# Kernel optimization log

Measured on AMD Instinct MI355X. Metric: run time of the kernel, lower is better.

Reference implementation:

```python
import jax, jax.numpy as jnp
import numpy as np

N, C, T, V = 16, 128, 128, 25
K, H, OC = 3, 8, 256          # kernel_size subsets, heads, out_channels
HOPMAX = 12                   # hop values in [0, 12); emb_table size HOPMAX
EPS_BN = 1e-5
EPS_NORM = 1e-4


def setup_inputs() -> dict:
    key = jax.random.key(0)
    ks = jax.random.split(key, 12)
    s = 0.05
    x = jax.random.normal(ks[0], (N, C, T, V), jnp.float32)
    hop = jax.random.randint(ks[1], (V, V), 0, HOPMAX)
    emb_table = jax.random.normal(ks[2], (K, H, HOPMAX), jnp.float32) * s
    # A initialized as identity (as in the module) plus small noise for nontrivial grads
    A = jnp.tile(jnp.eye(V, dtype=jnp.float32), (K, H, 1, 1)) \
        + jax.random.normal(ks[3], (K, H, V, V), jnp.float32) * s
    w_block = jax.random.normal(ks[4], (K * OC, C // H), jnp.float32) * s  # grouped 1x1 conv, groups=K*H
    b_block = jax.random.normal(ks[5], (K * OC,), jnp.float32) * s
    bn_gamma = jnp.ones((OC,), jnp.float32)
    bn_beta = jnp.zeros((OC,), jnp.float32)
    res_w = jax.random.normal(ks[6], (OC, C), jnp.float32) * s  # residual 1x1 conv
    res_b = jax.random.normal(ks[7], (OC,), jnp.float32) * s
    res_bn_gamma = jnp.ones((OC,), jnp.float32)
    res_bn_beta = jnp.zeros((OC,), jnp.float32)
    return {"x": x, "hop": hop, "emb_table": emb_table, "A": A,
            "w_block": w_block, "b_block": b_block,
            "bn_gamma": bn_gamma, "bn_beta": bn_beta,
            "res_w": res_w, "res_b": res_b,
            "res_bn_gamma": res_bn_gamma, "res_bn_beta": res_bn_beta}


def _batchnorm(x, gamma, beta):
    # training-mode BatchNorm2d: batch stats over (N, T, V), biased variance
    m = jnp.mean(x, axis=(0, 2, 3), keepdims=True)
    v = jnp.var(x, axis=(0, 2, 3), keepdims=True)
    xn = (x - m) * jax.lax.rsqrt(v + EPS_BN)
    return gamma[None, :, None, None] * xn + beta[None, :, None, None]


def _l2_col_norm(w):
    # torch.norm(w, p=2, dim=-2, keepdim=True) + 1e-4  (in-degree normalization)
    return jnp.sqrt(jnp.sum(w * w, axis=-2, keepdims=True)) + EPS_NORM


def reference(x, hop, emb_table, A, w_block, b_block, bn_gamma, bn_beta,
              res_w, res_b, res_bn_gamma, res_bn_beta):
    n, c, t, v = x.shape
    # residual: 1x1 TemporalConv2d + BN (in_channels != out_channels)
    res = jnp.einsum('nctv,oc->notv', x, res_w) + res_b[None, :, None, None]
    res = _batchnorm(res, res_bn_gamma, res_bn_beta)

    # hop-embedding gather -> [K, H, V, V]; fuse normalized B and A
    B = emb_table[:, :, hop]
    BnA = B / _l2_col_norm(B) + A / _l2_col_norm(A)

    # graph conv: einsum over joint dim v (broadcast over k)
    xh = x.reshape(n, H, c // H, t, v)                      # [N,H,C/H,T,V]
    y = jnp.einsum('nhctv,khvw->nkhctw', xh, BnA)           # [N,K,H,C/H,T,V]
    y = y.reshape(n, K * H, c // H, t, v)                   # groups = K*H

    # grouped 1x1 conv: per-group [C/H -> OC/H] GEMM
    wg = w_block.reshape(K * H, OC // H, c // H)
    out = jnp.einsum('ngctv,goc->ngotv', y, wg)             # [N,K*H,OC/H,T,V]
    out = out.reshape(n, K * OC, t, v) + b_block[None, :, None, None]

    # sum over the K kernel subsets
    out = out.reshape(n, K, OC, t, v).sum(axis=1)
    out = _batchnorm(out, bn_gamma, bn_beta)
    return jax.nn.relu(out + res)
```

## Files before the change

kernel.cpp:

```cpp
#include <hip/hip_runtime.h>
#include <stdint.h>

typedef __attribute__((ext_vector_type(8))) short short8;
typedef __attribute__((ext_vector_type(4))) float f32x4;

#define B_BNA    0ull
#define B_STATS  60416ull
#define B_RESW2  64512ull
#define B_PART   130048ull
#define B_E2     1178624ull
#define B_XB     7994368ull
#define B_MAIN   21625856ull
#define B_RES    47840256ull

#define NTV 51200.0f

__device__ __forceinline__ unsigned short f2bf(float f) {
    unsigned u = __float_as_uint(f);
    return (unsigned short)((u + 0x7fffu + ((u >> 16) & 1u)) >> 16);
}
__device__ __forceinline__ float bf2f(unsigned s) { return __uint_as_float(s << 16); }

__device__ __forceinline__ float wave_sum(float v) {
#pragma unroll
    for (int m = 1; m < 64; m <<= 1) v += __shfl_xor(v, m, 64);
    return v;
}

__global__ __launch_bounds__(256) void k_prep(const int* __restrict__ hop,
                                              const float* __restrict__ emb,
                                              const float* __restrict__ A,
                                              const float* __restrict__ res_w,
                                              float* __restrict__ bna,
                                              float* __restrict__ stats,
                                              unsigned short* __restrict__ resw2) {
    int g = blockIdx.x, tid = threadIdx.x;
    if (g < 24) {
        if (tid < 25) {
            int w = tid;
            float nb = 0.f, na = 0.f;
            for (int v = 0; v < 25; v++) {
                float e = emb[g*12 + hop[v*25 + w]];
                nb += e*e;
                float a = A[((size_t)g*25 + v)*25 + w];
                na += a*a;
            }
            nb = sqrtf(nb) + 1e-4f;
            na = sqrtf(na) + 1e-4f;
            for (int v = 0; v < 25; v++) {
                float e = emb[g*12 + hop[v*25 + w]];
                float a = A[((size_t)g*25 + v)*25 + w];
                bna[g*625 + v*25 + w] = e/nb + a/na;
            }
        }
    } else if (g == 24) {
#pragma unroll
        for (int i = 0; i < 4; i++) stats[i*256 + tid] = 0.f;
    } else {
        int base = (g - 25) * 4096 + tid * 16;
#pragma unroll
        for (int j = 0; j < 16; j++) resw2[base + j] = f2bf(res_w[base + j]);
    }
}

__global__ __launch_bounds__(256) void k_prep2(const float* __restrict__ w_block,
                                               const float* __restrict__ bna,
                                               unsigned short* __restrict__ E2) {
    __shared__ float bl[3*625];
    __shared__ float wl[3*64];
    int bid = blockIdx.x;
    int half = bid & 1, og = (bid >> 1) & 7, h = bid >> 4;
    int tid = threadIdx.x;

    for (int i = tid; i < 1875; i += 256) {
        int k3 = i / 625, j = i - k3*625;
        bl[i] = bna[(k3*8 + h)*625 + j];
    }
    if (tid < 192) {
        int k3 = tid >> 6, o = (tid >> 4) & 3, c = tid & 15;
        wl[tid] = w_block[(k3*256 + h*32 + og*4 + o)*16 + c];
    }
    __syncthreads();

    unsigned short* dst = E2 + (size_t)(h*8 + og)*53248;
    int e0 = half * 26624;
    for (int e = e0 + tid; e < e0 + 26624; e += 256) {
        int kc = e >> 12;
        int n  = (e >> 5) & 127;
        int kk = e & 31;
        int k  = kc*32 + kk;
        int o  = n >> 5, w = n & 31;
        float val = 0.f;
        if (k < 400 && w < 25) {
            int c = k / 25, v = k - c*25;
            val = wl[0*64 + o*16 + c] * bl[0*625 + v*25 + w]
                + wl[1*64 + o*16 + c] * bl[1*625 + v*25 + w]
                + wl[2*64 + o*16 + c] * bl[2*625 + v*25 + w];
        }
        dst[e] = f2bf(val);
    }
}

__global__ __launch_bounds__(256) void k_xprep(const float* __restrict__ x,
                                               unsigned short* __restrict__ xb) {
    int b = blockIdx.x;
    int n_ = b >> 7, t_ = b & 127;
    int tid = threadIdx.x;
    unsigned short* row = xb + (size_t)b * 3328;
    for (int idx = tid; idx < 3200; idx += 256) {
        int c = idx / 25, v = idx - c*25;
        float val = x[(((size_t)n_*128 + c)*128 + t_)*25 + v];
        row[(c >> 4)*416 + (c & 15)*25 + v] = f2bf(val);
    }
    if (tid < 128) row[(tid >> 4)*416 + 400 + (tid & 15)] = 0;
}

__global__ __launch_bounds__(256) void k_gc(const unsigned short* __restrict__ xb,
                                            const unsigned short* __restrict__ E2,
                                            unsigned short* __restrict__ mainp,
                                            float* __restrict__ stats) {
    __shared__ unsigned short Alds[128*32];
    __shared__ unsigned short Blds[128*32];
    int bid = blockIdx.x;
    int og = bid & 7, h = (bid >> 3) & 7, mt = bid >> 6;
    int tid = threadIdx.x;
    int lane = tid & 63, wave = tid >> 6;
    int wm = wave >> 1, wn = wave & 1;
    int lane15 = lane & 15, quad = lane >> 4;

    int srow = tid >> 1, shalf = tid & 1;
    const size_t abase = (size_t)(mt*128 + srow)*3328 + h*416 + shalf*16;
    const size_t bchunk0 = (size_t)(((h*8 + og)*13))*4096 + tid*16;

    f32x4 acc[4][4] = {};

    for (int kc = 0; kc < 13; kc++) {
        {
            const uint4* s = (const uint4*)(xb + abase + kc*32);
            uint4 a0 = s[0], a1 = s[1];
            *(uint4*)&Alds[srow*32 + shalf*16]     = a0;
            *(uint4*)&Alds[srow*32 + shalf*16 + 8] = a1;
        }
        {
            const uint4* s = (const uint4*)(E2 + bchunk0 + (size_t)kc*4096);
            uint4 b0 = s[0], b1 = s[1];
            *(uint4*)&Blds[tid*16]     = b0;
            *(uint4*)&Blds[tid*16 + 8] = b1;
        }
        __syncthreads();

        short8 af[4], bf[4];
#pragma unroll
        for (int i = 0; i < 4; i++) {
            af[i] = *(const short8*)&Alds[(wm*64 + i*16 + lane15)*32 + quad*8];
            bf[i] = *(const short8*)&Blds[(wn*64 + i*16 + lane15)*32 + quad*8];
        }
#pragma unroll
        for (int i = 0; i < 4; i++)
#pragma unroll
            for (int j = 0; j < 4; j++)
                acc[i][j] = __builtin_amdgcn_mfma_f32_16x16x32_bf16(af[i], bf[j], acc[i][j], 0, 0, 0);
        __syncthreads();
    }

    float s1[2] = {0.f, 0.f}, s2[2] = {0.f, 0.f};
#pragma unroll
    for (int j = 0; j < 4; j++) {
        int w = (j & 1)*16 + lane15;
        int p = j >> 1;
        if (w < 25) {
            int oc = h*32 + og*4 + wn*2 + p;
#pragma unroll
            for (int i = 0; i < 4; i++) {
                int mb = mt*128 + wm*64 + i*16 + quad*4;
#pragma unroll
                for (int r = 0; r < 4; r++) {
                    float val = acc[i][j][r];
                    mainp[(size_t)((mb + r)*256 + oc)*25 + w] = f2bf(val);
                    s1[p] += val;
                    s2[p] = fmaf(val, val, s2[p]);
                }
            }
        }
    }
#pragma unroll
    for (int p = 0; p < 2; p++) {
        float a = wave_sum(s1[p]);
        float b = wave_sum(s2[p]);
        if (lane == 0) {
            int oc = h*32 + og*4 + wn*2 + p;
            atomicAdd(&stats[oc], a);
            atomicAdd(&stats[256 + oc], b);
        }
    }
}

__global__ __launch_bounds__(256) void k_res(const float* __restrict__ x,
                                             const unsigned short* __restrict__ resw2,
                                             unsigned short* __restrict__ resp,
                                             float* __restrict__ stats) {
    __shared__ unsigned short Alds[128*32];
    __shared__ unsigned short Blds[128*32];
    int bid = blockIdx.x;
    int nt = bid & 1, mt = bid >> 1;
    int tid = threadIdx.x;
    int lane = tid & 63, wave = tid >> 6;
    int wm = wave >> 1, wn = wave & 1;
    int lane15 = lane & 15, quad = lane >> 4;

    int m2row = tid >> 1, shalf = tid & 1;
    int m2 = mt*128 + m2row;
    int bb = m2 / 25, vv = m2 - bb*25;
    int n_ = bb >> 7, t_ = bb & 127;
    const float* xbase = x + ((size_t)n_*128*128 + t_)*25 + vv;

    f32x4 acc[4][4] = {};

    for (int kc = 0; kc < 4; kc++) {
        {
            unsigned short tmp[16];
            int c0 = kc*32 + shalf*16;
#pragma unroll
            for (int j = 0; j < 16; j++)
                tmp[j] = f2bf(xbase[(size_t)(c0 + j)*3200]);
            unsigned pk[8];
#pragma unroll
            for (int q = 0; q < 8; q++)
                pk[q] = (unsigned)tmp[2*q] | ((unsigned)tmp[2*q+1] << 16);
            *(uint4*)&Alds[m2row*32 + shalf*16]     = make_uint4(pk[0], pk[1], pk[2], pk[3]);
            *(uint4*)&Alds[m2row*32 + shalf*16 + 8] = make_uint4(pk[4], pk[5], pk[6], pk[7]);
        }
        {
            const uint4* s = (const uint4*)(resw2 + (size_t)(nt*128 + m2row)*128 + kc*32 + shalf*16);
            uint4 b0 = s[0], b1 = s[1];
            *(uint4*)&Blds[m2row*32 + shalf*16]     = b0;
            *(uint4*)&Blds[m2row*32 + shalf*16 + 8] = b1;
        }
        __syncthreads();

        short8 af[4], bf[4];
#pragma unroll
        for (int i = 0; i < 4; i++) {
            af[i] = *(const short8*)&Alds[(wm*64 + i*16 + lane15)*32 + quad*8];
            bf[i] = *(const short8*)&Blds[(wn*64 + i*16 + lane15)*32 + quad*8];
        }
#pragma unroll
        for (int i = 0; i < 4; i++)
#pragma unroll
            for (int j = 0; j < 4; j++)
                acc[i][j] = __builtin_amdgcn_mfma_f32_16x16x32_bf16(af[i], bf[j], acc[i][j], 0, 0, 0);
        __syncthreads();
    }

#pragma unroll
    for (int j = 0; j < 4; j++) {
        int oc = nt*128 + wn*64 + j*16 + lane15;
        float s1 = 0.f, s2 = 0.f;
#pragma unroll
        for (int i = 0; i < 4; i++) {
            int m2b = mt*128 + wm*64 + i*16 + quad*4;
#pragma unroll
            for (int r = 0; r < 4; r++) {
                float val = acc[i][j][r];
                int m2e = m2b + r;
                int b = m2e / 25, v = m2e - b*25;
                resp[(size_t)(b*256 + oc)*25 + v] = f2bf(val);
                s1 += val;
                s2 = fmaf(val, val, s2);
            }
        }
        s1 += __shfl_xor(s1, 16, 64); s1 += __shfl_xor(s1, 32, 64);
        s2 += __shfl_xor(s2, 16, 64); s2 += __shfl_xor(s2, 32, 64);
        if (quad == 0) {
            atomicAdd(&stats[512 + oc], s1);
            atomicAdd(&stats[768 + oc], s2);
        }
    }
}

__global__ __launch_bounds__(256) void k_final(const float* __restrict__ bn_g,
                                               const float* __restrict__ bn_b,
                                               const float* __restrict__ rbn_g,
                                               const float* __restrict__ rbn_b,
                                               const float* __restrict__ stats,
                                               const unsigned short* __restrict__ mainp,
                                               const unsigned short* __restrict__ resp,
                                               float* __restrict__ out) {
    int b = blockIdx.x;
    int n_ = b >> 7, t_ = b & 127;
    int oc = threadIdx.x;
    const float inv = 1.f / NTV;
    float s1 = stats[oc],       s2 = stats[256 + oc];
    float r1 = stats[512 + oc], r2 = stats[768 + oc];
    float mm = s1*inv, vm = s2*inv - mm*mm;
    float mr = r1*inv, vr = r2*inv - mr*mr;
    float a1 = bn_g[oc]  * rsqrtf(vm + 1e-5f); float c1 = bn_b[oc]  - a1*mm;
    float a2 = rbn_g[oc] * rsqrtf(vr + 1e-5f); float c2 = rbn_b[oc] - a2*mr;

    const unsigned short* mrow = mainp + (size_t)(b*256 + oc)*25;
    const unsigned short* rrow = resp  + (size_t)(b*256 + oc)*25;
    float* op = out + ((size_t)(n_*256 + oc)*128 + t_)*25;
#pragma unroll
    for (int w = 0; w < 25; w++) {
        float val = fmaf(a1, bf2f(mrow[w]), c1) + fmaf(a2, bf2f(rrow[w]), c2);
        op[w] = fmaxf(val, 0.f);
    }
}

extern "C" void kernel_launch(void* const* d_in, const int* in_sizes, int n_in,
                              void* d_out, int out_size, void* d_ws, size_t ws_size,
                              hipStream_t stream) {
    const float* x        = (const float*)d_in[0];
    const int*   hop      = (const int*)  d_in[1];
    const float* emb      = (const float*)d_in[2];
    const float* A        = (const float*)d_in[3];
    const float* w_block  = (const float*)d_in[4];
    const float* bn_g     = (const float*)d_in[6];
    const float* bn_b     = (const float*)d_in[7];
    const float* res_w    = (const float*)d_in[8];
    const float* rbn_g    = (const float*)d_in[10];
    const float* rbn_b    = (const float*)d_in[11];
    float* out = (float*)d_out;

    char* ws = (char*)d_ws;
    float*          bna    = (float*)(ws + B_BNA);
    float*          stats  = (float*)(ws + B_STATS);
    unsigned short* resw2  = (unsigned short*)(ws + B_RESW2);
    unsigned short* E2     = (unsigned short*)(ws + B_E2);
    unsigned short* xb     = (unsigned short*)(ws + B_XB);
    unsigned short* mainp  = (unsigned short*)(ws + B_MAIN);
    unsigned short* resp   = (unsigned short*)(ws + B_RES);

    k_prep  <<<33,   256, 0, stream>>>(hop, emb, A, res_w, bna, stats, resw2);
    k_prep2 <<<128,  256, 0, stream>>>(w_block, bna, E2);
    k_xprep <<<2048, 256, 0, stream>>>(x, xb);
    k_gc    <<<1024, 256, 0, stream>>>(xb, E2, mainp, stats);
    k_res   <<<800,  256, 0, stream>>>(x, resw2, resp, stats);
    k_final <<<2048, 256, 0, stream>>>(bn_g, bn_b, rbn_g, rbn_b, stats, mainp, resp, out);
}
```

Before: 242.2 us.

## Merge prep kernels and GEMM kernels, use direct global-to-LDS loads

Folds k_prep2 and k_xprep into one launch, and k_gc and k_res into one launch split by block index, cutting the launch count from six to four. Tile staging now uses global_load_lds 16-byte direct copies into LDS instead of going through registers. The h/og block index mapping is swapped so neighbouring blocks share E2 tiles differently. In exchange, the merged GEMM kernel mixes two uneven workloads, and the direct LDS loads depend on a lane-to-address mapping that has to match the old tile layout.

Result: faster. 232.7 us (-3.9%).

```diff
diff --git a/kernel.cpp b/kernel.cpp
--- a/kernel.cpp
+++ b/kernel.cpp
@@ -25,6 +25,12 @@
 #pragma unroll
     for (int m = 1; m < 64; m <<= 1) v += __shfl_xor(v, m, 64);
     return v;
+}
+
+__device__ __forceinline__ void gl_lds16(const unsigned short* g, unsigned short* l) {
+    __builtin_amdgcn_global_load_lds(
+        (const __attribute__((address_space(1))) unsigned int*)g,
+        (__attribute__((address_space(3))) unsigned int*)l, 16, 0, 0);
 }
 
 __global__ __launch_bounds__(256) void k_prep(const int* __restrict__ hop,
@@ -63,217 +69,206 @@
     }
 }
 
-__global__ __launch_bounds__(256) void k_prep2(const float* __restrict__ w_block,
-                                               const float* __restrict__ bna,
-                                               unsigned short* __restrict__ E2) {
-    __shared__ float bl[3*625];
-    __shared__ float wl[3*64];
-    int bid = blockIdx.x;
-    int half = bid & 1, og = (bid >> 1) & 7, h = bid >> 4;
-    int tid = threadIdx.x;
-
-    for (int i = tid; i < 1875; i += 256) {
-        int k3 = i / 625, j = i - k3*625;
-        bl[i] = bna[(k3*8 + h)*625 + j];
+__global__ __launch_bounds__(256) void k_prep2x(const float* __restrict__ w_block,
+                                                const float* __restrict__ bna,
+                                                unsigned short* __restrict__ E2,
+                                                const float* __restrict__ x,
+                                                unsigned short* __restrict__ xb) {
+    int bid = blockIdx.x, tid = threadIdx.x;
+    if (bid < 128) {
+        __shared__ float bl[3*625];
+        __shared__ float wl[3*64];
+        int half = bid & 1, og = (bid >> 1) & 7, h = bid >> 4;
+
+        for (int i = tid; i < 1875; i += 256) {
+            int k3 = i / 625, j = i - k3*625;
+            bl[i] = bna[(k3*8 + h)*625 + j];
+        }
+        if (tid < 192) {
+            int k3 = tid >> 6, o = (tid >> 4) & 3, c = tid & 15;
+            wl[tid] = w_block[(k3*256 + h*32 + og*4 + o)*16 + c];
+        }
+        __syncthreads();
+
+        unsigned short* dst = E2 + (size_t)(h*8 + og)*53248;
+        int e0 = half * 26624;
+        for (int e = e0 + tid; e < e0 + 26624; e += 256) {
+            int kc = e >> 12;
+            int n  = (e >> 5) & 127;
+            int kk = e & 31;
+            int k  = kc*32 + kk;
+            int o  = n >> 5, w = n & 31;
+            float val = 0.f;
+            if (k < 400 && w < 25) {
+                int c = k / 25, v = k - c*25;
+                val = wl[0*64 + o*16 + c] * bl[0*625 + v*25 + w]
+                    + wl[1*64 + o*16 + c] * bl[1*625 + v*25 + w]
+                    + wl[2*64 + o*16 + c] * bl[2*625 + v*25 + w];
+            }
+            dst[e] = f2bf(val);
+        }
+    } else {
+        int b = bid - 128;
+        int n_ = b >> 7, t_ = b & 127;
+        unsigned short* row = xb + (size_t)b * 3328;
+        for (int idx = tid; idx < 3200; idx += 256) {
+            int c = idx / 25, v = idx - c*25;
+            float val = x[(((size_t)n_*128 + c)*128 + t_)*25 + v];
+            row[(c >> 4)*416 + (c & 15)*25 + v] = f2bf(val);
+        }
+        if (tid < 128) row[(tid >> 4)*416 + 400 + (tid & 15)] = 0;
     }
-    if (tid < 192) {
-        int k3 = tid >> 6, o = (tid >> 4) & 3, c = tid & 15;
-        wl[tid] = w_block[(k3*256 + h*32 + og*4 + o)*16 + c];
-    }
-    __syncthreads();
-
-    unsigned short* dst = E2 + (size_t)(h*8 + og)*53248;
-    int e0 = half * 26624;
-    for (int e = e0 + tid; e < e0 + 26624; e += 256) {
-        int kc = e >> 12;
-        int n  = (e >> 5) & 127;
-        int kk = e & 31;
-        int k  = kc*32 + kk;
-        int o  = n >> 5, w = n & 31;
-        float val = 0.f;
-        if (k < 400 && w < 25) {
-            int c = k / 25, v = k - c*25;
-            val = wl[0*64 + o*16 + c] * bl[0*625 + v*25 + w]
-                + wl[1*64 + o*16 + c] * bl[1*625 + v*25 + w]
-                + wl[2*64 + o*16 + c] * bl[2*625 + v*25 + w];
-        }
-        dst[e] = f2bf(val);
-    }
-}
-
-__global__ __launch_bounds__(256) void k_xprep(const float* __restrict__ x,
-                                               unsigned short* __restrict__ xb) {
-    int b = blockIdx.x;
-    int n_ = b >> 7, t_ = b & 127;
-    int tid = threadIdx.x;
-    unsigned short* row = xb + (size_t)b * 3328;
-    for (int idx = tid; idx < 3200; idx += 256) {
-        int c = idx / 25, v = idx - c*25;
-        float val = x[(((size_t)n_*128 + c)*128 + t_)*25 + v];
-        row[(c >> 4)*416 + (c & 15)*25 + v] = f2bf(val);
-    }
-    if (tid < 128) row[(tid >> 4)*416 + 400 + (tid & 15)] = 0;
-}
-
-__global__ __launch_bounds__(256) void k_gc(const unsigned short* __restrict__ xb,
+}
+
+__global__ __launch_bounds__(256) void k_mm(const unsigned short* __restrict__ xb,
                                             const unsigned short* __restrict__ E2,
                                             unsigned short* __restrict__ mainp,
+                                            const float* __restrict__ x,
+                                            const unsigned short* __restrict__ resw2,
+                                            unsigned short* __restrict__ resp,
                                             float* __restrict__ stats) {
     __shared__ unsigned short Alds[128*32];
     __shared__ unsigned short Blds[128*32];
-    int bid = blockIdx.x;
-    int og = bid & 7, h = (bid >> 3) & 7, mt = bid >> 6;
-    int tid = threadIdx.x;
+    int bid = blockIdx.x, tid = threadIdx.x;
     int lane = tid & 63, wave = tid >> 6;
     int wm = wave >> 1, wn = wave & 1;
     int lane15 = lane & 15, quad = lane >> 4;
 
-    int srow = tid >> 1, shalf = tid & 1;
-    const size_t abase = (size_t)(mt*128 + srow)*3328 + h*416 + shalf*16;
-    const size_t bchunk0 = (size_t)(((h*8 + og)*13))*4096 + tid*16;
-
-    f32x4 acc[4][4] = {};
-
-    for (int kc = 0; kc < 13; kc++) {
-        {
-            const uint4* s = (const uint4*)(xb + abase + kc*32);
-            uint4 a0 = s[0], a1 = s[1];
-            *(uint4*)&Alds[srow*32 + shalf*16]     = a0;
-            *(uint4*)&Alds[srow*32 + shalf*16 + 8] = a1;
-        }
-        {
-            const uint4* s = (const uint4*)(E2 + bchunk0 + (size_t)kc*4096);
-            uint4 b0 = s[0], b1 = s[1];
-            *(uint4*)&Blds[tid*16]     = b0;
-            *(uint4*)&Blds[tid*16 + 8] = b1;
-        }
-        __syncthreads();
-
-        short8 af[4], bf[4];
-#pragma unroll
-        for (int i = 0; i < 4; i++) {
-            af[i] = *(const short8*)&Alds[(wm*64 + i*16 + lane15)*32 + quad*8];
-            bf[i] = *(const short8*)&Blds[(wn*64 + i*16 + lane15)*32 + quad*8];
-        }
-#pragma unroll
-        for (int i = 0; i < 4; i++)
-#pragma unroll
-            for (int j = 0; j < 4; j++)
-                acc[i][j] = __builtin_amdgcn_mfma_f32_16x16x32_bf16(af[i], bf[j], acc[i][j], 0, 0, 0);
-        __syncthreads();
-    }
-
-    float s1[2] = {0.f, 0.f}, s2[2] = {0.f, 0.f};
-#pragma unroll
-    for (int j = 0; j < 4; j++) {
-        int w = (j & 1)*16 + lane15;
-        int p = j >> 1;
-        if (w < 25) {
-            int oc = h*32 + og*4 + wn*2 + p;
+    if (bid < 1024) {
+        int h = bid & 7, og = (bid >> 3) & 7, mt = bid >> 6;
+
+        const unsigned short* ag = xb + (size_t)(mt*128 + wave*32 + (lane>>2))*3328
+                                      + h*416 + (lane&3)*8;
+        const unsigned short* bg = E2 + (size_t)(h*8 + og)*53248 + wave*1024 + lane*8;
+        unsigned short* al = &Alds[wave*1024 + lane*8];
+        unsigned short* bl = &Blds[wave*1024 + lane*8];
+
+        f32x4 acc[4][4] = {};
+
+        for (int kc = 0; kc < 13; kc++) {
+            gl_lds16(ag,          al);
+            gl_lds16(ag + 53248,  al + 512);
+            gl_lds16(bg,          bl);
+            gl_lds16(bg + 512,    bl + 512);
+            ag += 32; bg += 4096;
+            __syncthreads();
+
+            short8 af[4], bf[4];
 #pragma unroll
             for (int i = 0; i < 4; i++) {
-                int mb = mt*128 + wm*64 + i*16 + quad*4;
+                af[i] = *(const short8*)&Alds[(wm*64 + i*16 + lane15)*32 + quad*8];
+                bf[i] = *(const short8*)&Blds[(wn*64 + i*16 + lane15)*32 + quad*8];
+            }
+#pragma unroll
+            for (int i = 0; i < 4; i++)
+#pragma unroll
+                for (int j = 0; j < 4; j++)
+                    acc[i][j] = __builtin_amdgcn_mfma_f32_16x16x32_bf16(af[i], bf[j], acc[i][j], 0, 0, 0);
+            __syncthreads();
+        }
+
+        float s1[2] = {0.f, 0.f}, s2[2] = {0.f, 0.f};
+#pragma unroll
+        for (int j = 0; j < 4; j++) {
+            int w = (j & 1)*16 + lane15;
+            int p = j >> 1;
+            if (w < 25) {
+                int oc = h*32 + og*4 + wn*2 + p;
+#pragma unroll
+                for (int i = 0; i < 4; i++) {
+                    int mb = mt*128 + wm*64 + i*16 + quad*4;
+#pragma unroll
+                    for (int r = 0; r < 4; r++) {
+                        float val = acc[i][j][r];
+                        mainp[(size_t)((mb + r)*256 + oc)*25 + w] = f2bf(val);
+                        s1[p] += val;
+                        s2[p] = fmaf(val, val, s2[p]);
+                    }
+                }
+            }
+        }
+#pragma unroll
+        for (int p = 0; p < 2; p++) {
+            float a = wave_sum(s1[p]);
+            float b = wave_sum(s2[p]);
+            if (lane == 0) {
+                int oc = h*32 + og*4 + wn*2 + p;
+                atomicAdd(&stats[oc], a);
+                atomicAdd(&stats[256 + oc], b);
+            }
+        }
+    } else {
+        int b2 = bid - 1024;
+        int nt = (b2 >= 400) ? 1 : 0;
+        int mt = b2 - nt*400;
+
+        int m2row = tid >> 1, shalf = tid & 1;
+        int m2 = mt*128 + m2row;
+        int bb = m2 / 25, vv = m2 - bb*25;
+        int n_ = bb >> 7, t_ = bb & 127;
+        const float* xbase = x + ((size_t)n_*128*128 + t_)*25 + vv;
+
+        const unsigned short* rbg = resw2 + (size_t)(nt*128 + wave*32 + (lane>>2))*128
+                                          + (lane&3)*8;
+        unsigned short* bl = &Blds[wave*1024 + lane*8];
+
+        f32x4 acc[4][4] = {};
+
+        for (int kc = 0; kc < 4; kc++) {
+            {
+                unsigned short tmp[16];
+                int c0 = kc*32 + shalf*16;
+#pragma unroll
+                for (int j = 0; j < 16; j++)
+                    tmp[j] = f2bf(xbase[(size_t)(c0 + j)*3200]);
+                unsigned pk[8];
+#pragma unroll
+                for (int q = 0; q < 8; q++)
+                    pk[q] = (unsigned)tmp[2*q] | ((unsigned)tmp[2*q+1] << 16);
+                *(uint4*)&Alds[m2row*32 + shalf*16]     = make_uint4(pk[0], pk[1], pk[2], pk[3]);
+                *(uint4*)&Alds[m2row*32 + shalf*16 + 8] = make_uint4(pk[4], pk[5], pk[6], pk[7]);
+            }
+            gl_lds16(rbg + kc*32,        bl);
+            gl_lds16(rbg + 2048 + kc*32, bl + 512);
+            __syncthreads();
+
+            short8 af[4], bf[4];
+#pragma unroll
+            for (int i = 0; i < 4; i++) {
+                af[i] = *(const short8*)&Alds[(wm*64 + i*16 + lane15)*32 + quad*8];
+                bf[i] = *(const short8*)&Blds[(wn*64 + i*16 + lane15)*32 + quad*8];
+            }
+#pragma unroll
+            for (int i = 0; i < 4; i++)
+#pragma unroll
+                for (int j = 0; j < 4; j++)
+                    acc[i][j] = __builtin_amdgcn_mfma_f32_16x16x32_bf16(af[i], bf[j], acc[i][j], 0, 0, 0);
+            __syncthreads();
+        }
+
+#pragma unroll
+        for (int j = 0; j < 4; j++) {
+            int oc = nt*128 + wn*64 + j*16 + lane15;
+            float s1 = 0.f, s2 = 0.f;
+#pragma unroll
+            for (int i = 0; i < 4; i++) {
+                int m2b = mt*128 + wm*64 + i*16 + quad*4;
 #pragma unroll
                 for (int r = 0; r < 4; r++) {
                     float val = acc[i][j][r];
-                    mainp[(size_t)((mb + r)*256 + oc)*25 + w] = f2bf(val);
-                    s1[p] += val;
-                    s2[p] = fmaf(val, val, s2[p]);
+                    int m2e = m2b + r;
+                    int b = m2e / 25, v = m2e - b*25;
+                    resp[(size_t)(b*256 + oc)*25 + v] = f2bf(val);
+                    s1 += val;
+                    s2 = fmaf(val, val, s2);
                 }
             }
-        }
-    }
-#pragma unroll
-    for (int p = 0; p < 2; p++) {
-        float a = wave_sum(s1[p]);
-        float b = wave_sum(s2[p]);
-        if (lane == 0) {
-            int oc = h*32 + og*4 + wn*2 + p;
-            atomicAdd(&stats[oc], a);
-            atomicAdd(&stats[256 + oc], b);
-        }
-    }
-}
-
-__global__ __launch_bounds__(256) void k_res(const float* __restrict__ x,
-                                             const unsigned short* __restrict__ resw2,
-                                             unsigned short* __restrict__ resp,
-                                             float* __restrict__ stats) {
-    __shared__ unsigned short Alds[128*32];
-    __shared__ unsigned short Blds[128*32];
-    int bid = blockIdx.x;
-    int nt = bid & 1, mt = bid >> 1;
-    int tid = threadIdx.x;
-    int lane = tid & 63, wave = tid >> 6;
-    int wm = wave >> 1, wn = wave & 1;
-    int lane15 = lane & 15, quad = lane >> 4;
-
-    int m2row = tid >> 1, shalf = tid & 1;
-    int m2 = mt*128 + m2row;
-    int bb = m2 / 25, vv = m2 - bb*25;
-    int n_ = bb >> 7, t_ = bb & 127;
-    const float* xbase = x + ((size_t)n_*128*128 + t_)*25 + vv;
-
-    f32x4 acc[4][4] = {};
-
-    for (int kc = 0; kc < 4; kc++) {
-        {
-            unsigned short tmp[16];
-            int c0 = kc*32 + shalf*16;
-#pragma unroll
-            for (int j = 0; j < 16; j++)
-                tmp[j] = f2bf(xbase[(size_t)(c0 + j)*3200]);
-            unsigned pk[8];
-#pragma unroll
-            for (int q = 0; q < 8; q++)
-                pk[q] = (unsigned)tmp[2*q] | ((unsigned)tmp[2*q+1] << 16);
-            *(uint4*)&Alds[m2row*32 + shalf*16]     = make_uint4(pk[0], pk[1], pk[2], pk[3]);
-            *(uint4*)&Alds[m2row*32 + shalf*16 + 8] = make_uint4(pk[4], pk[5], pk[6], pk[7]);
-        }
-        {
-            const uint4* s = (const uint4*)(resw2 + (size_t)(nt*128 + m2row)*128 + kc*32 + shalf*16);
-            uint4 b0 = s[0], b1 = s[1];
-            *(uint4*)&Blds[m2row*32 + shalf*16]     = b0;
-            *(uint4*)&Blds[m2row*32 + shalf*16 + 8] = b1;
-        }
-        __syncthreads();
-
-        short8 af[4], bf[4];
-#pragma unroll
-        for (int i = 0; i < 4; i++) {
-            af[i] = *(const short8*)&Alds[(wm*64 + i*16 + lane15)*32 + quad*8];
-            bf[i] = *(const short8*)&Blds[(wn*64 + i*16 + lane15)*32 + quad*8];
-        }
-#pragma unroll
-        for (int i = 0; i < 4; i++)
-#pragma unroll
-            for (int j = 0; j < 4; j++)
-                acc[i][j] = __builtin_amdgcn_mfma_f32_16x16x32_bf16(af[i], bf[j], acc[i][j], 0, 0, 0);
-        __syncthreads();
-    }
-
-#pragma unroll
-    for (int j = 0; j < 4; j++) {
-        int oc = nt*128 + wn*64 + j*16 + lane15;
-        float s1 = 0.f, s2 = 0.f;
-#pragma unroll
-        for (int i = 0; i < 4; i++) {
-            int m2b = mt*128 + wm*64 + i*16 + quad*4;
-#pragma unroll
-            for (int r = 0; r < 4; r++) {
-                float val = acc[i][j][r];
-                int m2e = m2b + r;
-                int b = m2e / 25, v = m2e - b*25;
-                resp[(size_t)(b*256 + oc)*25 + v] = f2bf(val);
-                s1 += val;
-                s2 = fmaf(val, val, s2);
-            }
-        }
-        s1 += __shfl_xor(s1, 16, 64); s1 += __shfl_xor(s1, 32, 64);
-        s2 += __shfl_xor(s2, 16, 64); s2 += __shfl_xor(s2, 32, 64);
-        if (quad == 0) {
-            atomicAdd(&stats[512 + oc], s1);
-            atomicAdd(&stats[768 + oc], s2);
+            s1 += __shfl_xor(s1, 16, 64); s1 += __shfl_xor(s1, 32, 64);
+            s2 += __shfl_xor(s2, 16, 64); s2 += __shfl_xor(s2, 32, 64);
+            if (quad == 0) {
+                atomicAdd(&stats[512 + oc], s1);
+                atomicAdd(&stats[768 + oc], s2);
+            }
         }
     }
 }
@@ -331,10 +326,8 @@
     unsigned short* mainp  = (unsigned short*)(ws + B_MAIN);
     unsigned short* resp   = (unsigned short*)(ws + B_RES);
 
-    k_prep  <<<33,   256, 0, stream>>>(hop, emb, A, res_w, bna, stats, resw2);
-    k_prep2 <<<128,  256, 0, stream>>>(w_block, bna, E2);
-    k_xprep <<<2048, 256, 0, stream>>>(x, xb);
-    k_gc    <<<1024, 256, 0, stream>>>(xb, E2, mainp, stats);
-    k_res   <<<800,  256, 0, stream>>>(x, resw2, resp, stats);
-    k_final <<<2048, 256, 0, stream>>>(bn_g, bn_b, rbn_g, rbn_b, stats, mainp, resp, out);
-}
+    k_prep   <<<33,   256, 0, stream>>>(hop, emb, A, res_w, bna, stats, resw2);
+    k_prep2x <<<2176, 256, 0, stream>>>(w_block, bna, E2, x, xb);
+    k_mm     <<<1824, 256, 0, stream>>>(xb, E2, mainp, x, resw2, resp, stats);
+    k_final  <<<2048, 256, 0, stream>>>(bn_g, bn_b, rbn_g, rbn_b, stats, mainp, resp, out);
+}
```
